# Kernel optimization log

Measured on AMD Instinct MI355X. Metric: run time of the kernel, lower is better.

Reference implementation:

```python
import jax, jax.numpy as jnp
import numpy as np

U = 3      # kronecker_partitions
DP = 128   # kronecker_subdim
K = 32     # top_k_slots
B = 64


def setup_inputs() -> dict:
    key = jax.random.key(0)
    z = jax.random.normal(key, (B, U * DP), dtype=jnp.float32)
    log_tau = jnp.zeros((1,), dtype=jnp.float32)  # learned temperature param
    return {"z": z, "log_tau": log_tau}


def reference(z, log_tau):
    b = z.shape[0]
    parts = z.reshape(b, U, DP)                      # [B, U, d_p]
    tau = jnp.exp(log_tau)
    probs = jax.nn.softmax(parts / tau, axis=-1)     # per-partition softmax
    # Kronecker (outer) product across partitions -> [B, d_p^U]
    addr = probs[:, 0]
    for u in range(1, U):  # static loop over U=3 partitions
        addr = (addr[:, :, None] * probs[:, u][:, None, :]).reshape(b, -1)
    weights, indices = jax.lax.top_k(addr, K)        # [B, K] each
    return indices, weights
```

## Files before the change

kernel.cpp:

```cpp
#include <hip/hip_runtime.h>
#include <math.h>

namespace {

constexpr int NU   = 3;
constexpr int DPN  = 128;
constexpr int TOPK = 32;
constexpr int NB   = 64;
constexpr int NCAND = 119;

__global__ __launch_bounds__(DPN) void kron_topk_kernel(
    const float* __restrict__ z, const float* __restrict__ log_tau,
    float* __restrict__ out) {
  const int row = blockIdx.x;
  const int tid = threadIdx.x;

  __shared__ float p[NU][DPN];
  __shared__ float red[DPN];
  __shared__ float sval[NU][TOPK];
  __shared__ int   sidx[NU][TOPK];
  __shared__ float cval[DPN];
  __shared__ int   cidx[DPN];
  __shared__ float aval[TOPK];
  __shared__ int   aidx[TOPK];

  const float tau = expf(log_tau[0]);

  for (int u = 0; u < NU; ++u) {
    float x = z[row * (NU * DPN) + u * DPN + tid] / tau;
    red[tid] = x;
    __syncthreads();
    for (int s = DPN / 2; s > 0; s >>= 1) {
      if (tid < s) red[tid] = fmaxf(red[tid], red[tid + s]);
      __syncthreads();
    }
    float m = red[0];
    __syncthreads();
    float e = expf(x - m);
    red[tid] = e;
    __syncthreads();
    for (int s = DPN / 2; s > 0; s >>= 1) {
      if (tid < s) red[tid] += red[tid + s];
      __syncthreads();
    }
    float denom = red[0];
    __syncthreads();
    p[u][tid] = e / denom;
    __syncthreads();
  }

  for (int u = 0; u < NU; ++u) {
    float v = p[u][tid];
    int rank = 0;
    for (int j = 0; j < DPN; ++j) {
      float w = p[u][j];
      rank += (w > v) || (w == v && j < tid);
    }
    if (rank < TOPK) { sval[u][rank] = v; sidx[u][rank] = tid; }
  }
  __syncthreads();

  if (tid < TOPK) { aval[tid] = sval[0][tid]; aidx[tid] = sidx[0][tid]; }
  __syncthreads();

  for (int u = 1; u < NU; ++u) {
    float v = -1.0f;
    int   idx = 0x7fffffff;
    if (tid < NCAND) {
      int t = tid, r = 0;
      while (true) {
        int cnt = TOPK / (r + 1);
        if (t < cnt) break;
        t -= cnt;
        ++r;
      }
      int s = t;
      v   = aval[r] * sval[u][s];
      idx = aidx[r] * DPN + sidx[u][s];
    }
    cval[tid] = v;
    cidx[tid] = idx;
    __syncthreads();

    int rank = 0;
    for (int j = 0; j < DPN; ++j) {
      float w = cval[j];
      rank += (w > v) || (w == v && cidx[j] < idx);
    }
    __syncthreads();
    if (rank < TOPK) { aval[rank] = v; aidx[rank] = idx; }
    __syncthreads();
  }

  if (tid < TOPK) {
    out[row * TOPK + tid]            = (float)aidx[tid];
    out[NB * TOPK + row * TOPK + tid] = aval[tid];
  }
}

}

extern "C" void kernel_launch(void* const* d_in, const int* in_sizes, int n_in,
                              void* d_out, int out_size, void* d_ws, size_t ws_size,
                              hipStream_t stream) {
  const float* z       = (const float*)d_in[0];
  const float* log_tau = (const float*)d_in[1];
  float* out           = (float*)d_out;
  hipLaunchKernelGGL(kron_topk_kernel, dim3(NB), dim3(DPN), 0, stream,
                     z, log_tau, out);
}
```

Baseline: 78.71 us.

## Use single-wavefront blocks with shuffle reductions for softmax and top-k

Shrinks each block from 128 threads to one 64-lane wavefront, with each lane handling two elements. The shared-memory tree reductions for softmax max and sum, which needed many barriers, become wave shuffle reductions. The rank-based top-k passes run two comparisons per lane. This removes most of the barrier and LDS round-trip latency in a tiny, latency-bound kernel, at the cost of halving the threads per block and doing twice the serial work per lane in the rank loops.

Result: slower. 86.88 us (+10.4%).

```diff
diff --git a/kernel.cpp b/kernel.cpp
--- a/kernel.cpp
+++ b/kernel.cpp
@@ -3,20 +3,19 @@
 
 namespace {
 
-constexpr int NU   = 3;
-constexpr int DPN  = 128;
-constexpr int TOPK = 32;
-constexpr int NB   = 64;
+constexpr int NU    = 3;
+constexpr int DPN   = 128;
+constexpr int TOPK  = 32;
+constexpr int NB    = 64;
 constexpr int NCAND = 119;
 
-__global__ __launch_bounds__(DPN) void kron_topk_kernel(
+__global__ __launch_bounds__(64) void kron_topk_kernel(
     const float* __restrict__ z, const float* __restrict__ log_tau,
     float* __restrict__ out) {
-  const int row = blockIdx.x;
-  const int tid = threadIdx.x;
+  const int row  = blockIdx.x;
+  const int lane = threadIdx.x;
 
   __shared__ float p[NU][DPN];
-  __shared__ float red[DPN];
   __shared__ float sval[NU][TOPK];
   __shared__ int   sidx[NU][TOPK];
   __shared__ float cval[DPN];
@@ -25,76 +24,86 @@
   __shared__ int   aidx[TOPK];
 
   const float tau = expf(log_tau[0]);
+  const float* zr = z + row * (NU * DPN);
+
+  float pv[NU][2];
+  for (int u = 0; u < NU; ++u) {
+    float x0 = zr[u * DPN + lane] / tau;
+    float x1 = zr[u * DPN + lane + 64] / tau;
+
+    float mm = fmaxf(x0, x1);
+    for (int d = 32; d > 0; d >>= 1) mm = fmaxf(mm, __shfl_xor(mm, d));
+    mm = __shfl(mm, 0);
+
+    float e0 = expf(x0 - mm);
+    float e1 = expf(x1 - mm);
+    float ss = e0 + e1;
+    for (int d = 32; d > 0; d >>= 1) ss += __shfl_xor(ss, d);
+    ss = __shfl(ss, 0);
+
+    pv[u][0] = e0 / ss;
+    pv[u][1] = e1 / ss;
+    p[u][lane]      = pv[u][0];
+    p[u][lane + 64] = pv[u][1];
+  }
+  __syncthreads();
 
   for (int u = 0; u < NU; ++u) {
-    float x = z[row * (NU * DPN) + u * DPN + tid] / tau;
-    red[tid] = x;
+    const float v0 = pv[u][0], v1 = pv[u][1];
+    int r0 = 0, r1 = 0;
+    for (int j = 0; j < DPN; ++j) {
+      float w = p[u][j];
+      r0 += (w > v0) || (w == v0 && j < lane);
+      r1 += (w > v1) || (w == v1 && j < lane + 64);
+    }
+    if (r0 < TOPK) { sval[u][r0] = v0; sidx[u][r0] = lane; }
+    if (r1 < TOPK) { sval[u][r1] = v1; sidx[u][r1] = lane + 64; }
+  }
+  __syncthreads();
+
+  if (lane < TOPK) { aval[lane] = sval[0][lane]; aidx[lane] = sidx[0][lane]; }
+  __syncthreads();
+
+  for (int u = 1; u < NU; ++u) {
+    for (int c = lane; c < DPN; c += 64) {
+      float v = -1.0f;
+      int idx = 0x7fffffff;
+      if (c < NCAND) {
+        int t = c, r = 0;
+        while (true) {
+          int cnt = TOPK / (r + 1);
+          if (t < cnt) break;
+          t -= cnt;
+          ++r;
+        }
+        v   = aval[r] * sval[u][t];
+        idx = aidx[r] * DPN + sidx[u][t];
+      }
+      cval[c] = v;
+      cidx[c] = idx;
+    }
     __syncthreads();
-    for (int s = DPN / 2; s > 0; s >>= 1) {
-      if (tid < s) red[tid] = fmaxf(red[tid], red[tid + s]);
-      __syncthreads();
+
+    const float v0 = cval[lane];
+    const float v1 = cval[lane + 64];
+    const int   i0 = cidx[lane];
+    const int   i1 = cidx[lane + 64];
+    int r0 = 0, r1 = 0;
+    for (int j = 0; j < DPN; ++j) {
+      float w = cval[j];
+      int  wi = cidx[j];
+      r0 += (w > v0) || (w == v0 && wi < i0);
+      r1 += (w > v1) || (w == v1 && wi < i1);
     }
-    float m = red[0];
     __syncthreads();
-    float e = expf(x - m);
-    red[tid] = e;
-    __syncthreads();
-    for (int s = DPN / 2; s > 0; s >>= 1) {
-      if (tid < s) red[tid] += red[tid + s];
-      __syncthreads();
-    }
-    float denom = red[0];
-    __syncthreads();
-    p[u][tid] = e / denom;
+    if (r0 < TOPK) { aval[r0] = v0; aidx[r0] = i0; }
+    if (r1 < TOPK) { aval[r1] = v1; aidx[r1] = i1; }
     __syncthreads();
   }
 
-  for (int u = 0; u < NU; ++u) {
-    float v = p[u][tid];
-    int rank = 0;
-    for (int j = 0; j < DPN; ++j) {
-      float w = p[u][j];
-      rank += (w > v) || (w == v && j < tid);
-    }
-    if (rank < TOPK) { sval[u][rank] = v; sidx[u][rank] = tid; }
-  }
-  __syncthreads();
-
-  if (tid < TOPK) { aval[tid] = sval[0][tid]; aidx[tid] = sidx[0][tid]; }
-  __syncthreads();
-
-  for (int u = 1; u < NU; ++u) {
-    float v = -1.0f;
-    int   idx = 0x7fffffff;
-    if (tid < NCAND) {
-      int t = tid, r = 0;
-      while (true) {
-        int cnt = TOPK / (r + 1);
-        if (t < cnt) break;
-        t -= cnt;
-        ++r;
-      }
-      int s = t;
-      v   = aval[r] * sval[u][s];
-      idx = aidx[r] * DPN + sidx[u][s];
-    }
-    cval[tid] = v;
-    cidx[tid] = idx;
-    __syncthreads();
-
-    int rank = 0;
-    for (int j = 0; j < DPN; ++j) {
-      float w = cval[j];
-      rank += (w > v) || (w == v && cidx[j] < idx);
-    }
-    __syncthreads();
-    if (rank < TOPK) { aval[rank] = v; aidx[rank] = idx; }
-    __syncthreads();
-  }
-
-  if (tid < TOPK) {
-    out[row * TOPK + tid]            = (float)aidx[tid];
-    out[NB * TOPK + row * TOPK + tid] = aval[tid];
+  if (lane < TOPK) {
+    out[row * TOPK + lane]             = (float)aidx[lane];
+    out[NB * TOPK + row * TOPK + lane] = aval[lane];
   }
 }
 
@@ -106,6 +115,6 @@
   const float* z       = (const float*)d_in[0];
   const float* log_tau = (const float*)d_in[1];
   float* out           = (float*)d_out;
-  hipLaunchKernelGGL(kron_topk_kernel, dim3(NB), dim3(DPN), 0, stream,
+  hipLaunchKernelGGL(kron_topk_kernel, dim3(NB), dim3(64), 0, stream,
                      z, log_tau, out);
 }
```

## Batch softmax reductions across partitions and vectorize rank-count loops

Applied to the files above, without the earlier changes.

The three per-partition softmax reductions are merged into one pass over a [3][128] shared buffer, so the barrier count drops from three sets of reduction barriers to one. The three rank-counting loops are fused into a single loop that reads float4 vectors from shared memory, and the candidate-merge rank loop is vectorized the same way. The candidate mapping is computed once up front, and the divide by tau is skipped when tau equals one. The kernel is tiny and launch-bound (64 blocks), so the gain may be small compared with fixed launch overhead.

Result: faster. 75.29 us (-4.3%).

```diff
diff --git a/kernel.cpp b/kernel.cpp
--- a/kernel.cpp
+++ b/kernel.cpp
@@ -3,10 +3,10 @@
 
 namespace {
 
-constexpr int NU   = 3;
-constexpr int DPN  = 128;
-constexpr int TOPK = 32;
-constexpr int NB   = 64;
+constexpr int NU    = 3;
+constexpr int DPN   = 128;
+constexpr int TOPK  = 32;
+constexpr int NB    = 64;
 constexpr int NCAND = 119;
 
 __global__ __launch_bounds__(DPN) void kron_topk_kernel(
@@ -15,48 +15,96 @@
   const int row = blockIdx.x;
   const int tid = threadIdx.x;
 
-  __shared__ float p[NU][DPN];
-  __shared__ float red[DPN];
+  __shared__ __align__(16) float p[NU][DPN];
+  __shared__ __align__(16) float red[NU][DPN];
   __shared__ float sval[NU][TOPK];
   __shared__ int   sidx[NU][TOPK];
-  __shared__ float cval[DPN];
-  __shared__ int   cidx[DPN];
+  __shared__ __align__(16) float cval[DPN];
+  __shared__ __align__(16) int   cidx[DPN];
   __shared__ float aval[TOPK];
   __shared__ int   aidx[TOPK];
 
+  const float* zr = z + row * (NU * DPN);
+  float x[NU];
+#pragma unroll
+  for (int u = 0; u < NU; ++u) x[u] = zr[u * DPN + tid];
   const float tau = expf(log_tau[0]);
 
-  for (int u = 0; u < NU; ++u) {
-    float x = z[row * (NU * DPN) + u * DPN + tid] / tau;
-    red[tid] = x;
-    __syncthreads();
-    for (int s = DPN / 2; s > 0; s >>= 1) {
-      if (tid < s) red[tid] = fmaxf(red[tid], red[tid + s]);
-      __syncthreads();
+  int rmap = 0, smap = 0;
+  const bool cact = tid < NCAND;
+  if (cact) {
+    int t = tid, r = 0;
+    while (true) {
+      int cnt = TOPK / (r + 1);
+      if (t < cnt) break;
+      t -= cnt;
+      ++r;
     }
-    float m = red[0];
-    __syncthreads();
-    float e = expf(x - m);
-    red[tid] = e;
-    __syncthreads();
-    for (int s = DPN / 2; s > 0; s >>= 1) {
-      if (tid < s) red[tid] += red[tid + s];
-      __syncthreads();
+    rmap = r;
+    smap = t;
+  }
+
+  if (tau != 1.0f) {
+#pragma unroll
+    for (int u = 0; u < NU; ++u) x[u] /= tau;
+  }
+#pragma unroll
+  for (int u = 0; u < NU; ++u) red[u][tid] = x[u];
+  __syncthreads();
+  for (int s = DPN / 2; s > 0; s >>= 1) {
+    if (tid < s) {
+#pragma unroll
+      for (int u = 0; u < NU; ++u)
+        red[u][tid] = fmaxf(red[u][tid], red[u][tid + s]);
     }
-    float denom = red[0];
-    __syncthreads();
-    p[u][tid] = e / denom;
     __syncthreads();
   }
+  float e[NU];
+#pragma unroll
+  for (int u = 0; u < NU; ++u) e[u] = expf(x[u] - red[u][0]);
+  __syncthreads();
+#pragma unroll
+  for (int u = 0; u < NU; ++u) red[u][tid] = e[u];
+  __syncthreads();
+  for (int s = DPN / 2; s > 0; s >>= 1) {
+    if (tid < s) {
+#pragma unroll
+      for (int u = 0; u < NU; ++u) red[u][tid] += red[u][tid + s];
+    }
+    __syncthreads();
+  }
+  float pv[NU];
+#pragma unroll
+  for (int u = 0; u < NU; ++u) {
+    pv[u] = e[u] / red[u][0];
+    p[u][tid] = pv[u];
+  }
+  __syncthreads();
 
-  for (int u = 0; u < NU; ++u) {
-    float v = p[u][tid];
-    int rank = 0;
-    for (int j = 0; j < DPN; ++j) {
-      float w = p[u][j];
-      rank += (w > v) || (w == v && j < tid);
+  {
+    int rk[NU] = {0, 0, 0};
+    const float4* p4_0 = reinterpret_cast<const float4*>(&p[0][0]);
+    const float4* p4_1 = reinterpret_cast<const float4*>(&p[1][0]);
+    const float4* p4_2 = reinterpret_cast<const float4*>(&p[2][0]);
+#pragma unroll 8
+    for (int jj = 0; jj < DPN / 4; ++jj) {
+      float4 w0 = p4_0[jj];
+      float4 w1 = p4_1[jj];
+      float4 w2 = p4_2[jj];
+      const float* w0e = &w0.x;
+      const float* w1e = &w1.x;
+      const float* w2e = &w2.x;
+#pragma unroll
+      for (int ee = 0; ee < 4; ++ee) {
+        int j = 4 * jj + ee;
+        rk[0] += (w0e[ee] > pv[0]) || (w0e[ee] == pv[0] && j < tid);
+        rk[1] += (w1e[ee] > pv[1]) || (w1e[ee] == pv[1] && j < tid);
+        rk[2] += (w2e[ee] > pv[2]) || (w2e[ee] == pv[2] && j < tid);
+      }
     }
-    if (rank < TOPK) { sval[u][rank] = v; sidx[u][rank] = tid; }
+#pragma unroll
+    for (int u = 0; u < NU; ++u)
+      if (rk[u] < TOPK) { sval[u][rk[u]] = pv[u]; sidx[u][rk[u]] = tid; }
   }
   __syncthreads();
 
@@ -65,27 +113,27 @@
 
   for (int u = 1; u < NU; ++u) {
     float v = -1.0f;
-    int   idx = 0x7fffffff;
-    if (tid < NCAND) {
-      int t = tid, r = 0;
-      while (true) {
-        int cnt = TOPK / (r + 1);
-        if (t < cnt) break;
-        t -= cnt;
-        ++r;
-      }
-      int s = t;
-      v   = aval[r] * sval[u][s];
-      idx = aidx[r] * DPN + sidx[u][s];
+    int idx = 0x7fffffff;
+    if (cact) {
+      v   = aval[rmap] * sval[u][smap];
+      idx = aidx[rmap] * DPN + sidx[u][smap];
     }
     cval[tid] = v;
     cidx[tid] = idx;
     __syncthreads();
 
     int rank = 0;
-    for (int j = 0; j < DPN; ++j) {
-      float w = cval[j];
-      rank += (w > v) || (w == v && cidx[j] < idx);
+    const float4* cv4 = reinterpret_cast<const float4*>(cval);
+    const int4*   ci4 = reinterpret_cast<const int4*>(cidx);
+#pragma unroll 8
+    for (int jj = 0; jj < DPN / 4; ++jj) {
+      float4 w4 = cv4[jj];
+      int4   i4 = ci4[jj];
+      const float* we = &w4.x;
+      const int*   ie = &i4.x;
+#pragma unroll
+      for (int ee = 0; ee < 4; ++ee)
+        rank += (we[ee] > v) || (we[ee] == v && ie[ee] < idx);
     }
     __syncthreads();
     if (rank < TOPK) { aval[rank] = v; aidx[rank] = idx; }
@@ -93,8 +141,8 @@
   }
 
   if (tid < TOPK) {
-    out[row * TOPK + tid]            = (float)aidx[tid];
-    out[NB * TOPK + row * TOPK + tid] = aval[tid];
+    out[row * TOPK + tid]              = (float)aidx[tid];
+    out[NB * TOPK + row * TOPK + tid]  = aval[tid];
   }
 }
 
```
